# Optimization experiments

Hardware: AMD Instinct MI355X
Metric: run time of the kernel (lower is better)

The kernel has to match this reference:

```python
import jax, jax.numpy as jnp
import numpy as np

NUM_NODES = 8192
NUM_EDGES = 262144
IN_C = 512
OUT_C = 512


def setup_inputs() -> dict:
    key = jax.random.key(0)
    k1, k2, k3, k4 = jax.random.split(key, 4)
    x = jax.random.normal(k1, (NUM_NODES, IN_C), dtype=jnp.float32)
    edge_index = jax.random.randint(k2, (2, NUM_EDGES), 0, NUM_NODES, dtype=jnp.int64)
    # nn.Linear params (W: [out, in], b: [out]) with kaiming-ish scale
    W = jax.random.normal(k3, (OUT_C, IN_C), dtype=jnp.float32) * (1.0 / np.sqrt(IN_C))
    b = jax.random.normal(k4, (OUT_C,), dtype=jnp.float32) * 0.01
    return {"x": x, "edge_index": edge_index, "W": W, "b": b}


def reference(x, edge_index, W, b):
    n = x.shape[0]
    # append self loops
    loop = jnp.arange(n, dtype=edge_index.dtype)
    rows = jnp.concatenate([edge_index[0], loop])
    cols = jnp.concatenate([edge_index[1], loop])
    # dense adjacency via scatter-set (duplicates collapse to 1.0, matching torch indexing assign)
    adj = jnp.zeros((n, n), dtype=jnp.float32).at[rows, cols].set(1.0)
    deg = adj.sum(axis=1)
    deg_inv_sqrt = jnp.where(deg > 0, jax.lax.rsqrt(jnp.maximum(deg, 1e-30)), 0.0)
    norm = deg_inv_sqrt[:, None] * adj * deg_inv_sqrt[None, :]
    h = x @ W.T + b            # [N, out_c]
    return norm @ h            # [N, out_c]
```

## Files before the change

kernel.cpp:

```cpp
#include <hip/hip_runtime.h>
#include <stdint.h>

#define N_NODES 8192
#define N_EDGES 262144
#define IN_C    512
#define OUT_C   512
#define MAX_DEG 512
#define X_ELEMS (N_NODES * IN_C)
#define W_ELEMS (OUT_C * IN_C)

typedef __attribute__((ext_vector_type(8))) short short8;
typedef __attribute__((ext_vector_type(4))) float f32x4;

__device__ inline uint16_t f2bf(float f) {
    uint32_t u = __float_as_uint(f);
    uint32_t r = (u + 0x7FFFu + ((u >> 16) & 1u)) >> 16;
    return (uint16_t)r;
}

__global__ __launch_bounds__(256) void convert_k(const float* __restrict__ x,
                                                 const float* __restrict__ W,
                                                 uint16_t* __restrict__ xb,
                                                 uint16_t* __restrict__ wb,
                                                 int* __restrict__ cnt) {
    int tid = blockIdx.x * 256 + threadIdx.x;
    if (tid < N_NODES) cnt[tid] = 0;
    int i = tid * 8;
    const float* src; uint16_t* dst;
    if (i < X_ELEMS) { src = x + i; dst = xb + i; }
    else             { src = W + (i - X_ELEMS); dst = wb + (i - X_ELEMS); }
    float4 v0 = *(const float4*)(src);
    float4 v1 = *(const float4*)(src + 4);
    ushort4 o0, o1;
    o0.x = f2bf(v0.x); o0.y = f2bf(v0.y); o0.z = f2bf(v0.z); o0.w = f2bf(v0.w);
    o1.x = f2bf(v1.x); o1.y = f2bf(v1.y); o1.z = f2bf(v1.z); o1.w = f2bf(v1.w);
    *(ushort4*)(dst)     = o0;
    *(ushort4*)(dst + 4) = o1;
}

__global__ __launch_bounds__(256) void scatter_k(const int* __restrict__ ei,
                                                 int* __restrict__ cnt,
                                                 uint16_t* __restrict__ nbr) {
    int t = blockIdx.x * 256 + threadIdx.x;
    int r, c;
    if (t < N_EDGES) {
        r = ei[t];
        c = ei[N_EDGES + t];
    } else if (t < N_EDGES + N_NODES) {
        r = t - N_EDGES; c = r;
    } else return;
    int pos = atomicAdd(&cnt[r], 1);
    if (pos < MAX_DEG) nbr[r * MAX_DEG + pos] = (uint16_t)c;
}

__global__ __launch_bounds__(256) void gemm_dedup_k(const uint16_t* __restrict__ xb,
                                                    const uint16_t* __restrict__ wb,
                                                    const float* __restrict__ bias,
                                                    uint16_t* __restrict__ h,
                                                    int* __restrict__ cnt,
                                                    uint16_t* __restrict__ nbr,
                                                    float* __restrict__ dis) {
    const int bid  = blockIdx.x;
    const int wave = threadIdx.x >> 6;
    const int lane = threadIdx.x & 63;

    if (bid < 512) {
        const int quad = lane >> 4;
        const int l16  = lane & 15;
        const int m_base = (bid >> 3) * 128 + (wave & 1) * 64;
        const int n_base = (bid & 7) * 64 + (wave >> 1) * 32;

        f32x4 acc[4][2];
        #pragma unroll
        for (int a = 0; a < 4; a++)
            #pragma unroll
            for (int s = 0; s < 2; s++) acc[a][s] = (f32x4){0.f, 0.f, 0.f, 0.f};

        #pragma unroll 2
        for (int k0 = 0; k0 < IN_C; k0 += 32) {
            short8 af[4], bf[2];
            #pragma unroll
            for (int a = 0; a < 4; a++)
                af[a] = *(const short8*)(xb + (m_base + a * 16 + l16) * IN_C + quad * 8 + k0);
            #pragma unroll
            for (int s = 0; s < 2; s++)
                bf[s] = *(const short8*)(wb + (n_base + s * 16 + l16) * IN_C + quad * 8 + k0);
            #pragma unroll
            for (int a = 0; a < 4; a++)
                #pragma unroll
                for (int s = 0; s < 2; s++)
                    acc[a][s] = __builtin_amdgcn_mfma_f32_16x16x32_bf16(af[a], bf[s], acc[a][s], 0, 0, 0);
        }
        #pragma unroll
        for (int s = 0; s < 2; s++) {
            int col = n_base + s * 16 + l16;
            float bv = bias[col];
            #pragma unroll
            for (int a = 0; a < 4; a++) {
                int row = m_base + a * 16 + quad * 4;
                #pragma unroll
                for (int r = 0; r < 4; r++)
                    h[(row + r) * OUT_C + col] = f2bf(acc[a][s][r] + bv);
            }
        }
    } else {
        __shared__ uint16_t buf[4][128];
        const int r = (bid - 512) * 4 + wave;

        int m0 = cnt[r]; if (m0 > 128) m0 = 128;
        for (int e = lane; e < m0; e += 64) buf[wave][e] = nbr[r * MAX_DEG + e];
        __syncthreads();

        bool k0 = false, k1 = false;
        uint16_t v0 = 0, v1 = 0;
        if (lane < m0) {
            v0 = buf[wave][lane]; k0 = true;
            for (int p = 0; p < lane; p++) if (buf[wave][p] == v0) { k0 = false; break; }
        }
        int e1 = lane + 64;
        if (e1 < m0) {
            v1 = buf[wave][e1]; k1 = true;
            for (int p = 0; p < e1; p++) if (buf[wave][p] == v1) { k1 = false; break; }
        }
        uint64_t b0 = __ballot(k0), b1 = __ballot(k1);
        uint64_t lt = (1ULL << lane) - 1ULL;
        int c0 = __popcll(b0);
        if (k0) nbr[r * MAX_DEG + __popcll(b0 & lt)] = v0;
        if (k1) nbr[r * MAX_DEG + c0 + __popcll(b1 & lt)] = v1;
        if (lane == 0) {
            int total = c0 + __popcll(b1);
            cnt[r] = total;
            dis[r] = rsqrtf((float)total);
        }
    }
}

__global__ __launch_bounds__(128) void aggregate_k(const int* __restrict__ cnt,
                                                   const uint16_t* __restrict__ nbr,
                                                   const float* __restrict__ dis,
                                                   const uint32_t* __restrict__ h2,
                                                   float* __restrict__ out) {
    const int i = blockIdx.x;
    const int half = blockIdx.y;
    int m = cnt[i]; if (m > MAX_DEG) m = MAX_DEG;

    __shared__ uint16_t jl[MAX_DEG];
    __shared__ float    dl[MAX_DEG];
    for (int t = threadIdx.x; t < m; t += 128) {
        uint16_t j = nbr[i * MAX_DEG + t];
        jl[t] = j;
        dl[t] = dis[j];
    }
    __syncthreads();

    const uint32_t* hp = h2 + half * 128 + threadIdx.x;
    float s0 = 0.f, s1 = 0.f;
    #pragma unroll 4
    for (int l = 0; l < m; l++) {
        uint32_t u = hp[(int)jl[l] * 256];
        float dj = dl[l];
        s0 += dj * __uint_as_float(u << 16);
        s1 += dj * __uint_as_float(u & 0xFFFF0000u);
    }
    float di = dis[i];
    int c = half * 256 + threadIdx.x * 2;
    float2 o = {di * s0, di * s1};
    *(float2*)(out + i * OUT_C + c) = o;
}

extern "C" void kernel_launch(void* const* d_in, const int* in_sizes, int n_in,
                              void* d_out, int out_size, void* d_ws, size_t ws_size,
                              hipStream_t stream) {
    const float* x  = (const float*)d_in[0];
    const int*   ei = (const int*)  d_in[1];
    const float* W  = (const float*)d_in[2];
    const float* b  = (const float*)d_in[3];
    float* out = (float*)d_out;
    char* ws = (char*)d_ws;

    const size_t CNT_OFF = 0;
    const size_t DIS_OFF = 32768;
    const size_t NBR_OFF = 65536;
    const size_t XB_OFF  = NBR_OFF + 8388608;
    const size_t WB_OFF  = XB_OFF + 8388608;
    const size_t H_OFF   = WB_OFF + 524288;
    int*      cnt = (int*)     (ws + CNT_OFF);
    float*    dis = (float*)   (ws + DIS_OFF);
    uint16_t* nbr = (uint16_t*)(ws + NBR_OFF);
    uint16_t* xb  = (uint16_t*)(ws + XB_OFF);
    uint16_t* wb  = (uint16_t*)(ws + WB_OFF);
    uint16_t* h   = (uint16_t*)(ws + H_OFF);

    convert_k<<<(X_ELEMS + W_ELEMS) / (256 * 8), 256, 0, stream>>>(x, W, xb, wb, cnt);

    scatter_k<<<(N_EDGES + N_NODES + 255) / 256, 256, 0, stream>>>(ei, cnt, nbr);

    gemm_dedup_k<<<512 + N_NODES / 4, 256, 0, stream>>>(xb, wb, b, h, cnt, nbr, dis);

    aggregate_k<<<dim3(N_NODES, 2), 128, 0, stream>>>(cnt, nbr, dis, (const uint32_t*)h, out);
}
```

Before: 142.9 us.

## Deduplicate edges with atomic bitmap and fuse scatter into GEMM launch

Replaces the per-row O(deg^2) shared-memory dedup pass with a global N×N bitmap: each edge does an atomicOr, and only the first setter appends to the neighbor list. The scatter work is merged into the GEMM kernel launch, removing one kernel, and degree rsqrt is computed on the fly in aggregation instead of being stored. It also remaps GEMM block order for better L2 reuse. The trade-off is zeroing an 8 MB bitmap in the convert kernel plus extra atomics, and the dedup cap of 128 is removed.

```diff
diff --git a/kernel.cpp b/kernel.cpp
--- a/kernel.cpp
+++ b/kernel.cpp
@@ -8,6 +8,7 @@
 #define MAX_DEG 512
 #define X_ELEMS (N_NODES * IN_C)
 #define W_ELEMS (OUT_C * IN_C)
+#define BM_WORDS (N_NODES * (N_NODES / 32))
 
 typedef __attribute__((ext_vector_type(8))) short short8;
 typedef __attribute__((ext_vector_type(4))) float f32x4;
@@ -22,9 +23,11 @@
                                                  const float* __restrict__ W,
                                                  uint16_t* __restrict__ xb,
                                                  uint16_t* __restrict__ wb,
-                                                 int* __restrict__ cnt) {
+                                                 int* __restrict__ cnt,
+                                                 uint4* __restrict__ bm) {
     int tid = blockIdx.x * 256 + threadIdx.x;
     if (tid < N_NODES) cnt[tid] = 0;
+    if (tid < BM_WORDS / 4) bm[tid] = make_uint4(0u, 0u, 0u, 0u);
     int i = tid * 8;
     const float* src; uint16_t* dst;
     if (i < X_ELEMS) { src = x + i; dst = xb + i; }
@@ -38,37 +41,24 @@
     *(ushort4*)(dst + 4) = o1;
 }
 
-__global__ __launch_bounds__(256) void scatter_k(const int* __restrict__ ei,
-                                                 int* __restrict__ cnt,
-                                                 uint16_t* __restrict__ nbr) {
-    int t = blockIdx.x * 256 + threadIdx.x;
-    int r, c;
-    if (t < N_EDGES) {
-        r = ei[t];
-        c = ei[N_EDGES + t];
-    } else if (t < N_EDGES + N_NODES) {
-        r = t - N_EDGES; c = r;
-    } else return;
-    int pos = atomicAdd(&cnt[r], 1);
-    if (pos < MAX_DEG) nbr[r * MAX_DEG + pos] = (uint16_t)c;
-}
-
-__global__ __launch_bounds__(256) void gemm_dedup_k(const uint16_t* __restrict__ xb,
-                                                    const uint16_t* __restrict__ wb,
-                                                    const float* __restrict__ bias,
-                                                    uint16_t* __restrict__ h,
-                                                    int* __restrict__ cnt,
-                                                    uint16_t* __restrict__ nbr,
-                                                    float* __restrict__ dis) {
-    const int bid  = blockIdx.x;
-    const int wave = threadIdx.x >> 6;
-    const int lane = threadIdx.x & 63;
-
+__global__ __launch_bounds__(256) void gemm_scatter_k(const uint16_t* __restrict__ xb,
+                                                      const uint16_t* __restrict__ wb,
+                                                      const float* __restrict__ bias,
+                                                      uint16_t* __restrict__ h,
+                                                      const int* __restrict__ ei,
+                                                      int* __restrict__ cnt,
+                                                      uint16_t* __restrict__ nbr,
+                                                      uint32_t* __restrict__ bm) {
+    const int bid = blockIdx.x;
     if (bid < 512) {
+        const int wave = threadIdx.x >> 6;
+        const int lane = threadIdx.x & 63;
         const int quad = lane >> 4;
         const int l16  = lane & 15;
-        const int m_base = (bid >> 3) * 128 + (wave & 1) * 64;
-        const int n_base = (bid & 7) * 64 + (wave >> 1) * 32;
+        const int mrow = (bid & 7) * 8 + (bid >> 6);
+        const int ncol = (bid >> 3) & 7;
+        const int m_base = mrow * 128 + (wave & 1) * 64;
+        const int n_base = ncol * 64 + (wave >> 1) * 32;
 
         f32x4 acc[4][2];
         #pragma unroll
@@ -104,40 +94,26 @@
             }
         }
     } else {
-        __shared__ uint16_t buf[4][128];
-        const int r = (bid - 512) * 4 + wave;
-
-        int m0 = cnt[r]; if (m0 > 128) m0 = 128;
-        for (int e = lane; e < m0; e += 64) buf[wave][e] = nbr[r * MAX_DEG + e];
-        __syncthreads();
-
-        bool k0 = false, k1 = false;
-        uint16_t v0 = 0, v1 = 0;
-        if (lane < m0) {
-            v0 = buf[wave][lane]; k0 = true;
-            for (int p = 0; p < lane; p++) if (buf[wave][p] == v0) { k0 = false; break; }
-        }
-        int e1 = lane + 64;
-        if (e1 < m0) {
-            v1 = buf[wave][e1]; k1 = true;
-            for (int p = 0; p < e1; p++) if (buf[wave][p] == v1) { k1 = false; break; }
-        }
-        uint64_t b0 = __ballot(k0), b1 = __ballot(k1);
-        uint64_t lt = (1ULL << lane) - 1ULL;
-        int c0 = __popcll(b0);
-        if (k0) nbr[r * MAX_DEG + __popcll(b0 & lt)] = v0;
-        if (k1) nbr[r * MAX_DEG + c0 + __popcll(b1 & lt)] = v1;
-        if (lane == 0) {
-            int total = c0 + __popcll(b1);
-            cnt[r] = total;
-            dis[r] = rsqrtf((float)total);
+        int t = (bid - 512) * 256 + threadIdx.x;
+        int r, c;
+        if (t < N_EDGES) {
+            r = ei[t];
+            c = ei[N_EDGES + t];
+        } else if (t < N_EDGES + N_NODES) {
+            r = t - N_EDGES; c = r;
+        } else return;
+        uint32_t w   = (uint32_t)r * (uint32_t)(N_NODES / 32) + ((uint32_t)c >> 5);
+        uint32_t bit = 1u << (c & 31);
+        uint32_t old = atomicOr(&bm[w], bit);
+        if (!(old & bit)) {
+            int pos = atomicAdd(&cnt[r], 1);
+            if (pos < MAX_DEG) nbr[r * MAX_DEG + pos] = (uint16_t)c;
         }
     }
 }
 
 __global__ __launch_bounds__(128) void aggregate_k(const int* __restrict__ cnt,
                                                    const uint16_t* __restrict__ nbr,
-                                                   const float* __restrict__ dis,
                                                    const uint32_t* __restrict__ h2,
                                                    float* __restrict__ out) {
     const int i = blockIdx.x;
@@ -149,7 +125,7 @@
     for (int t = threadIdx.x; t < m; t += 128) {
         uint16_t j = nbr[i * MAX_DEG + t];
         jl[t] = j;
-        dl[t] = dis[j];
+        dl[t] = rsqrtf((float)cnt[j]);
     }
     __syncthreads();
 
@@ -162,7 +138,7 @@
         s0 += dj * __uint_as_float(u << 16);
         s1 += dj * __uint_as_float(u & 0xFFFF0000u);
     }
-    float di = dis[i];
+    float di = rsqrtf((float)m);
     int c = half * 256 + threadIdx.x * 2;
     float2 o = {di * s0, di * s1};
     *(float2*)(out + i * OUT_C + c) = o;
@@ -179,23 +155,22 @@
     char* ws = (char*)d_ws;
 
     const size_t CNT_OFF = 0;
-    const size_t DIS_OFF = 32768;
-    const size_t NBR_OFF = 65536;
+    const size_t BM_OFF  = 32768;
+    const size_t NBR_OFF = BM_OFF + 8388608;
     const size_t XB_OFF  = NBR_OFF + 8388608;
     const size_t WB_OFF  = XB_OFF + 8388608;
     const size_t H_OFF   = WB_OFF + 524288;
     int*      cnt = (int*)     (ws + CNT_OFF);
-    float*    dis = (float*)   (ws + DIS_OFF);
+    uint32_t* bm  = (uint32_t*)(ws + BM_OFF);
     uint16_t* nbr = (uint16_t*)(ws + NBR_OFF);
     uint16_t* xb  = (uint16_t*)(ws + XB_OFF);
     uint16_t* wb  = (uint16_t*)(ws + WB_OFF);
     uint16_t* h   = (uint16_t*)(ws + H_OFF);
 
-    convert_k<<<(X_ELEMS + W_ELEMS) / (256 * 8), 256, 0, stream>>>(x, W, xb, wb, cnt);
+    convert_k<<<(X_ELEMS + W_ELEMS) / (256 * 8), 256, 0, stream>>>(x, W, xb, wb, cnt, (uint4*)bm);
 
-    scatter_k<<<(N_EDGES + N_NODES + 255) / 256, 256, 0, stream>>>(ei, cnt, nbr);
+    gemm_scatter_k<<<512 + (N_EDGES + N_NODES + 255) / 256, 256, 0, stream>>>(
+        xb, wb, b, h, ei, cnt, nbr, bm);
 
-    gemm_dedup_k<<<512 + N_NODES / 4, 256, 0, stream>>>(xb, wb, b, h, cnt, nbr, dis);
-
-    aggregate_k<<<dim3(N_NODES, 2), 128, 0, stream>>>(cnt, nbr, dis, (const uint32_t*)h, out);
+    aggregate_k<<<dim3(N_NODES, 2), 128, 0, stream>>>(cnt, nbr, (const uint32_t*)h, out);
 }
```

Result: faster. 135.4 us (-5.2%).
